# Kernel optimization log

Measured on AMD Instinct MI355X. Metric: run time of the kernel, lower is better.

Reference implementation:

```python
import jax, jax.numpy as jnp
import numpy as np

N = 100000      # nodes
E = 1600000     # edges
F_IN = 128      # feature_dim
H = 128         # hidden_dim
OUT = 40        # out_dim


def setup_inputs() -> dict:
    key = jax.random.key(0)
    ks = jax.random.split(key, 8)
    x = jax.random.normal(ks[0], (N, F_IN), dtype=jnp.float32)
    edge_index = jax.random.randint(ks[1], (2, E), 0, N)
    def lin(k, fan_in, fan_out):
        kw, kb = jax.random.split(k)
        s = 1.0 / np.sqrt(fan_in)
        W = jax.random.uniform(kw, (fan_in, fan_out), jnp.float32, -s, s)
        b = jax.random.uniform(kb, (fan_out,), jnp.float32, -s, s)
        return W, b
    W1, b1 = lin(ks[2], F_IN, H)
    W2, b2 = lin(ks[3], H, H)
    Wc, bc = lin(ks[4], H, OUT)
    return {"x": x, "W1": W1, "b1": b1, "W2": W2, "b2": b2,
            "Wc": Wc, "bc": bc, "edge_index": edge_index}


def gcn_conv(x, W, b, src, dst, n):
    # GCNConv: D^{-1/2} (A + I) D^{-1/2} X W + b  (self loops already in src/dst)
    h = x @ W                                            # [n, out]
    deg = jax.ops.segment_sum(jnp.ones(src.shape[0], h.dtype), dst,
                              num_segments=n)            # [n]
    dinv = jnp.where(deg > 0, jax.lax.rsqrt(deg), 0.0)
    norm = dinv[src] * dinv[dst]                         # [E+n]
    msg = h[src] * norm[:, None]                         # gather + scale
    out = jax.ops.segment_sum(msg, dst, num_segments=n)  # scatter-add
    return out + b


def reference(x, W1, b1, W2, b2, Wc, bc, edge_index):
    loops = jnp.arange(N, dtype=edge_index.dtype)
    src = jnp.concatenate([edge_index[0], loops])
    dst = jnp.concatenate([edge_index[1], loops])
    # mode=0, eval mode: dropout is identity
    out1 = jax.nn.relu(gcn_conv(x, W1, b1, src, dst, N))
    out2 = jax.nn.relu(gcn_conv(out1, W2, b2, src, dst, N))
    return (out2 + out1) @ Wc + bc
```

## Files before the change

kernel.cpp:

```cpp
#include <hip/hip_runtime.h>
#include <stdint.h>


#define HID 128
#define OUTD 40
#define BSH 8
#define BCAP 6144
#define CAPSH 13
#define EPB 8192
#define NBMAX 512

typedef __attribute__((ext_vector_type(8))) short short8;
typedef __attribute__((ext_vector_type(4))) float f32x4;
typedef __attribute__((ext_vector_type(2))) float f32x2;

__device__ inline uint16_t f32_to_bf16(float f) {
    uint32_t u = __float_as_uint(f);
    uint32_t r = u + 0x7FFFu + ((u >> 16) & 1u);
    return (uint16_t)(r >> 16);
}
__device__ inline uint32_t pack_bf16x2(float lo, float hi) {
    return (uint32_t)f32_to_bf16(lo) | ((uint32_t)f32_to_bf16(hi) << 16);
}
__device__ inline float bf_lo(uint32_t u) { return __uint_as_float(u << 16); }
__device__ inline float bf_hi(uint32_t u) { return __uint_as_float(u & 0xFFFF0000u); }
__device__ inline f32x2 up2(uint32_t u) {
    f32x2 r;
    r.x = __uint_as_float(u << 16);
    r.y = __uint_as_float(u & 0xFFFF0000u);
    return r;
}

__global__ __launch_bounds__(256) void gnn_scatter_wsw_k(const int* __restrict__ edges,
                                                         int* __restrict__ pcur,
                                                         uint32_t* __restrict__ pairbuf,
                                                         const float* __restrict__ W1,
                                                         const float* __restrict__ W2,
                                                         uint16_t* __restrict__ w1s,
                                                         uint16_t* __restrict__ w2s,
                                                         int E, int NB, int nEB) {
    if ((int)blockIdx.x >= nEB) {
        int wb = blockIdx.x - nEB;
        const float* W = (wb < 8) ? W1 : W2;
        uint16_t* O = (wb < 8) ? w1s : w2s;
        int t = (wb & 7) * 256 + threadIdx.x;
        int lane = t & 63;
        int ksct = t >> 6;
        int nn = (ksct >> 2) * 16 + (lane & 15);
        int k0 = (ksct & 3) * 32 + (lane >> 4) * 8;
        uint32_t d[4];
#pragma unroll
        for (int j = 0; j < 4; ++j)
            d[j] = pack_bf16x2(W[(size_t)(k0 + 2 * j) * HID + nn],
                               W[(size_t)(k0 + 2 * j + 1) * HID + nn]);
        *(uint4*)(O + (size_t)t * 8) = make_uint4(d[0], d[1], d[2], d[3]);
        return;
    }
    __shared__ int hist[NBMAX];
    int e0 = blockIdx.x * EPB;
    int e1 = min(E, e0 + EPB);
    for (int b = threadIdx.x; b < NB; b += 256) hist[b] = 0;
    __syncthreads();
    for (int e = e0 + threadIdx.x; e < e1; e += 256)
        atomicAdd(&hist[edges[E + e] >> BSH], 1);
    __syncthreads();
    for (int b = threadIdx.x; b < NB; b += 256) {
        int c = hist[b];
        hist[b] = (c > 0) ? (atomicAdd(&pcur[b], c) + (b << CAPSH)) : 0;
    }
    __syncthreads();
    for (int e = e0 + threadIdx.x; e < e1; e += 256) {
        int src = edges[e];
        int dst = edges[E + e];
        int pos = atomicAdd(&hist[dst >> BSH], 1);
        pairbuf[pos] = ((uint32_t)(dst & 255) << 24) | (uint32_t)src;
    }
}

__global__ __launch_bounds__(256) void gnn_build_csr_k(const uint32_t* __restrict__ pairbuf,
                                                       const int* __restrict__ pcur,
                                                       int* __restrict__ rowptr,
                                                       float* __restrict__ dinv,
                                                       int* __restrict__ colidx, int n) {
    __shared__ int red[256];
    __shared__ int deg[256];
    __shared__ int scn[256];
    __shared__ int colbuf[BCAP];
    int b = blockIdx.x;
    int t = threadIdx.x;

    int part = 0;
    for (int i = t; i < b; i += 256) part += pcur[i];
    red[t] = part;
    __syncthreads();
    for (int off = 128; off > 0; off >>= 1) {
        if (t < off) red[t] += red[t + off];
        __syncthreads();
    }
    const int segbeg = red[0] + (b << BSH);

    int nb0 = b << BSH;
    int nb1 = min(n, nb0 + 256);
    int nn = nb1 - nb0;
    int npairs = pcur[b];
    int seglen = npairs + nn;
    int pairbeg = b << CAPSH;

    deg[t] = 0;
    __syncthreads();
    for (int p = t; p < npairs; p += 256)
        atomicAdd(&deg[pairbuf[pairbeg + p] >> 24], 1);
    __syncthreads();

    int d = (t < nn) ? deg[t] : 0;
    int v = (t < nn) ? d + 1 : 0;
    scn[t] = v;
    __syncthreads();
    for (int off = 1; off < 256; off <<= 1) {
        int x = 0;
        if (t >= off) x = scn[t - off];
        __syncthreads();
        if (t >= off) scn[t] += x;
        __syncthreads();
    }
    int rel = scn[t] - v;
    if (t < nn) {
        rowptr[nb0 + t + 1] = segbeg + scn[t];
        dinv[nb0 + t] = rsqrtf((float)(d + 1));
    }
    if (t == 0) rowptr[nb0] = segbeg;
    __syncthreads();

    if (seglen <= BCAP) {
        if (t < nn) {
            colbuf[rel] = nb0 + t;
            deg[t] = rel + 1;
        }
        __syncthreads();
        for (int p = t; p < npairs; p += 256) {
            uint32_t pr = pairbuf[pairbeg + p];
            int pos = atomicAdd(&deg[pr >> 24], 1);
            colbuf[pos] = (int)(pr & 0xFFFFFFu);
        }
        __syncthreads();
        for (int i = t; i < seglen; i += 256)
            colidx[segbeg + i] = colbuf[i];
    } else {
        if (t < nn) {
            colidx[segbeg + rel] = nb0 + t;
            deg[t] = rel + 1;
        }
        __syncthreads();
        for (int p = t; p < npairs; p += 256) {
            uint32_t pr = pairbuf[pairbeg + p];
            int pos = atomicAdd(&deg[pr >> 24], 1);
            colidx[segbeg + pos] = (int)(pr & 0xFFFFFFu);
        }
    }
}


template <bool ABF16>
__global__ __launch_bounds__(256) void gnn_gemm_mfma_k(const void* __restrict__ Aptr,
                                                       const uint32_t* __restrict__ Wsw,
                                                       const float* __restrict__ dinv,
                                                       uint16_t* __restrict__ outh, int n) {
    int wave = threadIdx.x >> 6;
    int lane = threadIdx.x & 63;
    int m = lane & 15;
    int q = lane >> 4;
    int row0 = blockIdx.x * 64 + wave * 16;
    int arow = min(row0 + m, n - 1);

    f32x4 acc[8];
#pragma unroll
    for (int i = 0; i < 8; ++i) acc[i] = (f32x4){0.f, 0.f, 0.f, 0.f};

#pragma unroll
    for (int ks = 0; ks < 4; ++ks) {
        short8 a;
        if (ABF16) {
            const uint16_t* Ab = (const uint16_t*)Aptr;
            uint4 u = *(const uint4*)(Ab + (size_t)arow * HID + ks * 32 + q * 8);
            a = __builtin_bit_cast(short8, u);
        } else {
            const float* Af = (const float*)Aptr + (size_t)arow * HID + ks * 32 + q * 8;
            uint4 u0 = *(const uint4*)(Af);
            uint4 u1 = *(const uint4*)(Af + 4);
            uint4 p;
            p.x = pack_bf16x2(__uint_as_float(u0.x), __uint_as_float(u0.y));
            p.y = pack_bf16x2(__uint_as_float(u0.z), __uint_as_float(u0.w));
            p.z = pack_bf16x2(__uint_as_float(u1.x), __uint_as_float(u1.y));
            p.w = pack_bf16x2(__uint_as_float(u1.z), __uint_as_float(u1.w));
            a = __builtin_bit_cast(short8, p);
        }
#pragma unroll
        for (int ct = 0; ct < 8; ++ct) {
            uint4 bu = *(const uint4*)(Wsw + ((size_t)(ct * 4 + ks) * 64 + lane) * 4);
            short8 bfr = __builtin_bit_cast(short8, bu);
            acc[ct] = __builtin_amdgcn_mfma_f32_16x16x32_bf16(a, bfr, acc[ct], 0, 0, 0);
        }
    }

    float dv[4];
#pragma unroll
    for (int r = 0; r < 4; ++r) dv[r] = dinv[min(row0 + q * 4 + r, n - 1)];

#pragma unroll
    for (int ct = 0; ct < 8; ++ct) {
#pragma unroll
        for (int r = 0; r < 4; ++r) {
            int rr = row0 + q * 4 + r;
            if (rr < n)
                outh[(size_t)rr * HID + ct * 16 + m] = f32_to_bf16(acc[ct][r] * dv[r]);
        }
    }
}


template <bool FUSE_HEAD>
__global__ __launch_bounds__(256) void gnn_aggregate_k(const uint4* __restrict__ h4,
                                const int* __restrict__ rowptr,
                                const int* __restrict__ colidx, const float* __restrict__ dinv,
                                const float* __restrict__ bias,
                                const uint16_t* __restrict__ skipb,
                                uint16_t* __restrict__ outsh,
                                const float* __restrict__ wc,
                                const float* __restrict__ bc,
                                float* __restrict__ outf, int n) {
    __shared__ float srow[4][HID];
    int wv = threadIdx.x >> 6;
    int node = blockIdx.x * 4 + wv;
    if (node >= n) return;
    int lane = threadIdx.x & 63;
    int g = lane >> 4;
    int sub = lane & 15;
    int beg = rowptr[node];
    int end = rowptr[node + 1];
    f32x2 acc2[4];
#pragma unroll
    for (int i = 0; i < 4; ++i) acc2[i] = (f32x2){0.f, 0.f};
    int e = beg;
    for (; e + 15 < end; e += 16) {
        int j0 = colidx[e + g];
        int j1 = colidx[e + 4 + g];
        int j2 = colidx[e + 8 + g];
        int j3 = colidx[e + 12 + g];
        uint4 u0 = h4[(size_t)j0 * 16 + sub];
        uint4 u1 = h4[(size_t)j1 * 16 + sub];
        uint4 u2 = h4[(size_t)j2 * 16 + sub];
        uint4 u3 = h4[(size_t)j3 * 16 + sub];
        acc2[0] += up2(u0.x); acc2[1] += up2(u0.y); acc2[2] += up2(u0.z); acc2[3] += up2(u0.w);
        acc2[0] += up2(u1.x); acc2[1] += up2(u1.y); acc2[2] += up2(u1.z); acc2[3] += up2(u1.w);
        acc2[0] += up2(u2.x); acc2[1] += up2(u2.y); acc2[2] += up2(u2.z); acc2[3] += up2(u2.w);
        acc2[0] += up2(u3.x); acc2[1] += up2(u3.y); acc2[2] += up2(u3.z); acc2[3] += up2(u3.w);
    }
    for (; e + 3 < end; e += 4) {
        int j = colidx[e + g];
        uint4 u = h4[(size_t)j * 16 + sub];
        acc2[0] += up2(u.x); acc2[1] += up2(u.y); acc2[2] += up2(u.z); acc2[3] += up2(u.w);
    }
    if (g < end - e) {
        int j = colidx[e + g];
        uint4 u = h4[(size_t)j * 16 + sub];
        acc2[0] += up2(u.x); acc2[1] += up2(u.y); acc2[2] += up2(u.z); acc2[3] += up2(u.w);
    }
    float a8[8];
#pragma unroll
    for (int i = 0; i < 4; ++i) { a8[2 * i] = acc2[i].x; a8[2 * i + 1] = acc2[i].y; }
#pragma unroll
    for (int k = 0; k < 8; ++k) {
        a8[k] += __shfl_xor(a8[k], 16, 64);
        a8[k] += __shfl_xor(a8[k], 32, 64);
    }
    if (lane < 32) {
        int half = lane >> 4;
        int col = sub * 8 + half * 4;
        float di = dinv[node];
        float4 bv = *(const float4*)(bias + col);
        float o0 = fmaxf(di * a8[half * 4 + 0] + bv.x, 0.0f);
        float o1 = fmaxf(di * a8[half * 4 + 1] + bv.y, 0.0f);
        float o2 = fmaxf(di * a8[half * 4 + 2] + bv.z, 0.0f);
        float o3 = fmaxf(di * a8[half * 4 + 3] + bv.w, 0.0f);
        if (skipb) {
            uint2 sv = *(const uint2*)(skipb + (size_t)node * HID + col);
            o0 += bf_lo(sv.x); o1 += bf_hi(sv.x);
            o2 += bf_lo(sv.y); o3 += bf_hi(sv.y);
        }
        if (!FUSE_HEAD) {
            uint2 sh;
            sh.x = pack_bf16x2(o0, o1);
            sh.y = pack_bf16x2(o2, o3);
            *(uint2*)(outsh + (size_t)node * HID + col) = sh;
        } else {
            *(float4*)&srow[wv][col] = make_float4(o0, o1, o2, o3);
        }
    }
    if (FUSE_HEAD) {
        if (lane < OUTD) {
            float acc = bc[lane];
            const float4* s4 = (const float4*)srow[wv];
#pragma unroll 4
            for (int k4 = 0; k4 < HID / 4; ++k4) {
                float4 sv = s4[k4];
                acc += sv.x * wc[(size_t)(k4 * 4 + 0) * OUTD + lane];
                acc += sv.y * wc[(size_t)(k4 * 4 + 1) * OUTD + lane];
                acc += sv.z * wc[(size_t)(k4 * 4 + 2) * OUTD + lane];
                acc += sv.w * wc[(size_t)(k4 * 4 + 3) * OUTD + lane];
            }
            outf[(size_t)node * OUTD + lane] = acc;
        }
    }
}


extern "C" void kernel_launch(void* const* d_in, const int* in_sizes, int n_in,
                              void* d_out, int out_size, void* d_ws, size_t ws_size,
                              hipStream_t stream) {
    const int N = in_sizes[0] / HID;
    const int E = in_sizes[7] / 2;

    const float* x  = (const float*)d_in[0];
    const float* W1 = (const float*)d_in[1];
    const float* b1 = (const float*)d_in[2];
    const float* W2 = (const float*)d_in[3];
    const float* b2 = (const float*)d_in[4];
    const float* Wc = (const float*)d_in[5];
    const float* bc = (const float*)d_in[6];
    const int* edges = (const int*)d_in[7];
    float* out = (float*)d_out;

    char* w = (char*)d_ws;
    auto alloc = [&](size_t bytes) -> char* {
        char* p = w;
        w += (bytes + 255) & ~(size_t)255;
        return p;
    };
    uint16_t* hbuf  = (uint16_t*)alloc((size_t)N * HID * 2);
    uint16_t* bufBh = (uint16_t*)alloc((size_t)N * HID * 2);
    int*   rowptr  = (int*)alloc((size_t)(N + 1) * 4);
    int*   colidx  = (int*)alloc((size_t)(E + N) * 4);
    float* dinv    = (float*)alloc((size_t)N * 4);
    int*   pcur    = (int*)alloc(512 * 4);
    uint16_t* w1s  = (uint16_t*)alloc(HID * HID * 2);
    uint16_t* w2s  = (uint16_t*)alloc(HID * HID * 2);

    uint32_t* pairbuf = (uint32_t*)hbuf;

    const int NB = (N + 255) >> BSH;
    const int nEB = (E + EPB - 1) / EPB;

    hipMemsetAsync(pcur, 0, 512 * 4, stream);

    gnn_scatter_wsw_k<<<nEB + 16, 256, 0, stream>>>(edges, pcur, pairbuf,
                                                    W1, W2, w1s, w2s, E, NB, nEB);
    gnn_build_csr_k<<<NB, 256, 0, stream>>>(pairbuf, pcur, rowptr, dinv, colidx, N);

    gnn_gemm_mfma_k<false><<<(N + 63) / 64, 256, 0, stream>>>(x, (const uint32_t*)w1s, dinv, hbuf, N);
    gnn_aggregate_k<false><<<(N + 3) / 4, 256, 0, stream>>>((const uint4*)hbuf, rowptr, colidx,
                                                            dinv, b1, nullptr, bufBh,
                                                            nullptr, nullptr, nullptr, N);
    gnn_gemm_mfma_k<true><<<(N + 63) / 64, 256, 0, stream>>>(bufBh, (const uint32_t*)w2s, dinv, hbuf, N);
    gnn_aggregate_k<true><<<(N + 3) / 4, 256, 0, stream>>>((const uint4*)hbuf, rowptr, colidx,
                                                           dinv, b2, bufBh, nullptr,
                                                           Wc, bc, out, N);
}
```

Baseline: 366.6 us.

## Unfuse classifier head into separate MFMA GEMM kernel with split-bf16 weights

```diff
diff --git a/kernel.cpp b/kernel.cpp
--- a/kernel.cpp
+++ b/kernel.cpp
@@ -24,6 +24,7 @@
 }
 __device__ inline float bf_lo(uint32_t u) { return __uint_as_float(u << 16); }
 __device__ inline float bf_hi(uint32_t u) { return __uint_as_float(u & 0xFFFF0000u); }
+__device__ inline float bf16_val(uint16_t h) { return __uint_as_float((uint32_t)h << 16); }
 __device__ inline f32x2 up2(uint32_t u) {
     f32x2 r;
     r.x = __uint_as_float(u << 16);
@@ -36,9 +37,33 @@
                                                          uint32_t* __restrict__ pairbuf,
                                                          const float* __restrict__ W1,
                                                          const float* __restrict__ W2,
+                                                         const float* __restrict__ Wc,
                                                          uint16_t* __restrict__ w1s,
                                                          uint16_t* __restrict__ w2s,
+                                                         uint16_t* __restrict__ wcs,
                                                          int E, int NB, int nEB) {
+    if ((int)blockIdx.x >= nEB + 16) {
+        int ct = blockIdx.x - nEB - 16;
+        int t = threadIdx.x;
+        int lane = t & 63;
+        int ks = t >> 6;
+        int col = ct * 16 + (lane & 15);
+        int k0 = ks * 32 + (lane >> 4) * 8;
+        uint32_t dh[4], dl[4];
+#pragma unroll
+        for (int j = 0; j < 4; ++j) {
+            float wa = (col < OUTD) ? Wc[(size_t)(k0 + 2 * j) * OUTD + col] : 0.f;
+            float wb = (col < OUTD) ? Wc[(size_t)(k0 + 2 * j + 1) * OUTD + col] : 0.f;
+            uint16_t ha = f32_to_bf16(wa), hb = f32_to_bf16(wb);
+            float la = wa - bf16_val(ha), lb = wb - bf16_val(hb);
+            dh[j] = (uint32_t)ha | ((uint32_t)hb << 16);
+            dl[j] = pack_bf16x2(la, lb);
+        }
+        size_t ent = (size_t)(ct * 256 + t) * 8;
+        *(uint4*)(wcs + ent) = make_uint4(dh[0], dh[1], dh[2], dh[3]);
+        *(uint4*)(wcs + 6144 + ent) = make_uint4(dl[0], dl[1], dl[2], dl[3]);
+        return;
+    }
     if ((int)blockIdx.x >= nEB) {
         int wb = blockIdx.x - nEB;
         const float* W = (wb < 8) ? W1 : W2;
@@ -218,19 +243,13 @@
 }
 
 
-template <bool FUSE_HEAD>
 __global__ __launch_bounds__(256) void gnn_aggregate_k(const uint4* __restrict__ h4,
                                 const int* __restrict__ rowptr,
                                 const int* __restrict__ colidx, const float* __restrict__ dinv,
                                 const float* __restrict__ bias,
                                 const uint16_t* __restrict__ skipb,
-                                uint16_t* __restrict__ outsh,
-                                const float* __restrict__ wc,
-                                const float* __restrict__ bc,
-                                float* __restrict__ outf, int n) {
-    __shared__ float srow[4][HID];
-    int wv = threadIdx.x >> 6;
-    int node = blockIdx.x * 4 + wv;
+                                uint16_t* __restrict__ outsh, int n) {
+    int node = blockIdx.x * 4 + (threadIdx.x >> 6);
     if (node >= n) return;
     int lane = threadIdx.x & 63;
     int g = lane >> 4;
@@ -287,28 +306,55 @@
             o0 += bf_lo(sv.x); o1 += bf_hi(sv.x);
             o2 += bf_lo(sv.y); o3 += bf_hi(sv.y);
         }
-        if (!FUSE_HEAD) {
-            uint2 sh;
-            sh.x = pack_bf16x2(o0, o1);
-            sh.y = pack_bf16x2(o2, o3);
-            *(uint2*)(outsh + (size_t)node * HID + col) = sh;
-        } else {
-            *(float4*)&srow[wv][col] = make_float4(o0, o1, o2, o3);
-        }
-    }
-    if (FUSE_HEAD) {
-        if (lane < OUTD) {
-            float acc = bc[lane];
-            const float4* s4 = (const float4*)srow[wv];
-#pragma unroll 4
-            for (int k4 = 0; k4 < HID / 4; ++k4) {
-                float4 sv = s4[k4];
-                acc += sv.x * wc[(size_t)(k4 * 4 + 0) * OUTD + lane];
-                acc += sv.y * wc[(size_t)(k4 * 4 + 1) * OUTD + lane];
-                acc += sv.z * wc[(size_t)(k4 * 4 + 2) * OUTD + lane];
-                acc += sv.w * wc[(size_t)(k4 * 4 + 3) * OUTD + lane];
+        uint2 sh;
+        sh.x = pack_bf16x2(o0, o1);
+        sh.y = pack_bf16x2(o2, o3);
+        *(uint2*)(outsh + (size_t)node * HID + col) = sh;
+    }
+}
+
+
+__global__ __launch_bounds__(256) void gnn_final_k(const uint16_t* __restrict__ sumh,
+                                                   const uint32_t* __restrict__ Wcs,
+                                                   const float* __restrict__ bc,
+                                                   float* __restrict__ out, int n) {
+    int wave = threadIdx.x >> 6;
+    int lane = threadIdx.x & 63;
+    int m = lane & 15;
+    int q = lane >> 4;
+    int row0 = blockIdx.x * 64 + wave * 16;
+    int arow = min(row0 + m, n - 1);
+
+    f32x4 acc[3];
+#pragma unroll
+    for (int i = 0; i < 3; ++i) acc[i] = (f32x4){0.f, 0.f, 0.f, 0.f};
+
+#pragma unroll
+    for (int ks = 0; ks < 4; ++ks) {
+        uint4 u = *(const uint4*)(sumh + (size_t)arow * HID + ks * 32 + q * 8);
+        short8 a = __builtin_bit_cast(short8, u);
+#pragma unroll
+        for (int ct = 0; ct < 3; ++ct) {
+            uint4 bh = *(const uint4*)(Wcs + ((size_t)(ct * 4 + ks) * 64 + lane) * 4);
+            uint4 bl = *(const uint4*)(Wcs + 3072 + ((size_t)(ct * 4 + ks) * 64 + lane) * 4);
+            short8 fh = __builtin_bit_cast(short8, bh);
+            short8 fl = __builtin_bit_cast(short8, bl);
+            acc[ct] = __builtin_amdgcn_mfma_f32_16x16x32_bf16(a, fh, acc[ct], 0, 0, 0);
+            acc[ct] = __builtin_amdgcn_mfma_f32_16x16x32_bf16(a, fl, acc[ct], 0, 0, 0);
+        }
+    }
+
+#pragma unroll
+    for (int ct = 0; ct < 3; ++ct) {
+        int col = ct * 16 + m;
+        if (col < OUTD) {
+            float bcv = bc[col];
+#pragma unroll
+            for (int r = 0; r < 4; ++r) {
+                int rr = row0 + q * 4 + r;
+                if (rr < n)
+                    out[(size_t)rr * OUTD + col] = acc[ct][r] + bcv;
             }
-            outf[(size_t)node * OUTD + lane] = acc;
         }
     }
 }
@@ -344,6 +390,7 @@
     int*   pcur    = (int*)alloc(512 * 4);
     uint16_t* w1s  = (uint16_t*)alloc(HID * HID * 2);
     uint16_t* w2s  = (uint16_t*)alloc(HID * HID * 2);
+    uint16_t* wcs  = (uint16_t*)alloc(2 * 6144 * 2);
 
     uint32_t* pairbuf = (uint32_t*)hbuf;
 
@@ -352,16 +399,15 @@
 
     hipMemsetAsync(pcur, 0, 512 * 4, stream);
 
-    gnn_scatter_wsw_k<<<nEB + 16, 256, 0, stream>>>(edges, pcur, pairbuf,
-                                                    W1, W2, w1s, w2s, E, NB, nEB);
+    gnn_scatter_wsw_k<<<nEB + 19, 256, 0, stream>>>(edges, pcur, pairbuf,
+                                                    W1, W2, Wc, w1s, w2s, wcs, E, NB, nEB);
     gnn_build_csr_k<<<NB, 256, 0, stream>>>(pairbuf, pcur, rowptr, dinv, colidx, N);
 
     gnn_gemm_mfma_k<false><<<(N + 63) / 64, 256, 0, stream>>>(x, (const uint32_t*)w1s, dinv, hbuf, N);
-    gnn_aggregate_k<false><<<(N + 3) / 4, 256, 0, stream>>>((const uint4*)hbuf, rowptr, colidx,
-                                                            dinv, b1, nullptr, bufBh,
-                                                            nullptr, nullptr, nullptr, N);
+    gnn_aggregate_k<<<(N + 3) / 4, 256, 0, stream>>>((const uint4*)hbuf, rowptr, colidx,
+                                                     dinv, b1, nullptr, bufBh, N);
     gnn_gemm_mfma_k<true><<<(N + 63) / 64, 256, 0, stream>>>(bufBh, (const uint32_t*)w2s, dinv, hbuf, N);
-    gnn_aggregate_k<true><<<(N + 3) / 4, 256, 0, stream>>>((const uint4*)hbuf, rowptr, colidx,
-                                                           dinv, b2, bufBh, nullptr,
-                                                           Wc, bc, out, N);
-}
+    gnn_aggregate_k<<<(N + 3) / 4, 256, 0, stream>>>((const uint4*)hbuf, rowptr, colidx,
+                                                     dinv, b2, bufBh, bufBh, N);
+    gnn_final_k<<<(N + 63) / 64, 256, 0, stream>>>(bufBh, (const uint32_t*)wcs, bc, out, N);
+}
```

New measurement: 324.4 us (median of 2 runs). 11.5% less time.
